# Kernel optimization log

Hardware: AMD Instinct MI355X
Metric: run time of the kernel (lower is better)

The kernel has to match this reference:

```python
import jax, jax.numpy as jnp
import numpy as np
from jax import lax

B, N, C = 4, 3072, 512
SAMPLE_RATIO = 0.25
CLUSTER_NUM = int(np.ceil(N * SAMPLE_RATIO))  # 768, static (mask=None, no 'r')
K = 5  # self.k, since k <= cluster_num


def setup_inputs() -> dict:
    key = jax.random.key(0)
    k1, = jax.random.split(key, 1)
    x = jax.random.normal(k1, (B, N, C), dtype=jnp.float32)
    # idx_token starts as identity mapping per batch (standard TCFormer init)
    idx_token = jnp.tile(jnp.arange(N, dtype=jnp.int32)[None, :], (B, 1))
    agg_weight = jnp.ones((B, N, 1), dtype=jnp.float32)
    return {"x": x, "idx_token": idx_token, "agg_weight": agg_weight}


def _cluster_dpc_knn(x):
    # runs under no_grad in torch -> stop_gradient here
    xs = lax.stop_gradient(x).astype(jnp.float32)
    sq = jnp.sum(xs * xs, axis=-1)  # [B,N]
    d2 = sq[:, :, None] + sq[:, None, :] - 2.0 * jnp.einsum('bnc,bmc->bnm', xs, xs)
    dist = jnp.sqrt(jnp.maximum(d2, 0.0)) / jnp.sqrt(jnp.float32(C))  # cdist / C**0.5
    # k nearest (smallest) distances
    neg_nearest, _ = lax.top_k(-dist, K)
    dist_nearest = -neg_nearest  # [B,N,K]
    density = jnp.exp(-jnp.mean(dist_nearest ** 2, axis=-1))
    density = density + jax.random.uniform(jax.random.key(42), density.shape, dtype=density.dtype) * 1e-6
    mask = (density[:, None, :] > density[:, :, None]).astype(x.dtype)  # [B,N,N]
    dist_max = jnp.max(dist.reshape(B, -1), axis=-1)[:, None, None]
    dist_min = jnp.min(dist * mask + dist_max * (1.0 - mask), axis=-1)  # [B,N]
    score = dist_min * density
    _, index_down = lax.top_k(score, CLUSTER_NUM)  # [B,cluster]
    # gather rows of dist at cluster centers, assign each token to nearest center
    dmat = jnp.take_along_axis(dist, index_down[:, :, None], axis=1)  # [B,cluster,N]
    idx_cluster = jnp.argmin(dmat, axis=1).astype(jnp.int32)  # [B,N]
    # force centers to map to their own cluster id
    idx_cluster = idx_cluster.at[jnp.arange(B)[:, None], index_down].set(
        jnp.broadcast_to(jnp.arange(CLUSTER_NUM, dtype=jnp.int32)[None, :], (B, CLUSTER_NUM)))
    return idx_cluster


def reference(x, idx_token, agg_weight):
    idx_cluster = _cluster_dpc_knn(x)
    # merge_tokens
    token_weight = jnp.ones((B, N, 1), dtype=x.dtype)
    idx = idx_cluster + jnp.arange(B, dtype=jnp.int32)[:, None] * CLUSTER_NUM  # [B,N]
    idx_flat = idx.reshape(-1)
    all_weight = jax.ops.segment_sum(token_weight.reshape(-1), idx_flat,
                                     num_segments=B * CLUSTER_NUM) + 1e-6  # [B*cluster]
    norm_weight = token_weight / all_weight[idx_flat].reshape(B, N, 1)  # [B,N,1]
    x_merged = jax.ops.segment_sum((x * norm_weight).reshape(B * N, C), idx_flat,
                                   num_segments=B * CLUSTER_NUM).reshape(B, CLUSTER_NUM, C)
    idx_token_new = jnp.take_along_axis(idx_cluster, idx_token, axis=1)  # [B,N]
    weight_t = jnp.take_along_axis(norm_weight, idx_token[:, :, None], axis=1)  # [B,N,1]
    agg_weight_new = agg_weight * weight_t
    return x_merged, agg_weight_new, idx_token_new, idx_cluster
```

## Files before the change

### kernel.cpp

```cpp
#include <hip/hip_runtime.h>
#include <math.h>
#include <float.h>

constexpr int B  = 4;
constexpr int N  = 3072;
constexpr int C  = 512;
constexpr int CL = 768;

typedef unsigned short u16;
typedef __attribute__((ext_vector_type(8))) short s16x8;
typedef __attribute__((ext_vector_type(4))) float f32x4;

__device__ __forceinline__ unsigned rotl32(unsigned v, int d) { return (v << d) | (v >> (32 - d)); }

__device__ inline void threefry2x32(unsigned k0, unsigned k1, unsigned c0, unsigned c1,
                                    unsigned& o0, unsigned& o1) {
  unsigned ks0 = k0, ks1 = k1, ks2 = 0x1BD11BDAu ^ k0 ^ k1;
  unsigned x0 = c0 + ks0, x1 = c1 + ks1;
#define TF_RND(r) { x0 += x1; x1 = rotl32(x1, (r)); x1 ^= x0; }
  TF_RND(13) TF_RND(15) TF_RND(26) TF_RND(6)  x0 += ks1; x1 += ks2 + 1u;
  TF_RND(17) TF_RND(29) TF_RND(16) TF_RND(24) x0 += ks2; x1 += ks0 + 2u;
  TF_RND(13) TF_RND(15) TF_RND(26) TF_RND(6)  x0 += ks0; x1 += ks1 + 3u;
  TF_RND(17) TF_RND(29) TF_RND(16) TF_RND(24) x0 += ks1; x1 += ks2 + 4u;
  TF_RND(13) TF_RND(15) TF_RND(26) TF_RND(6)  x0 += ks2; x1 += ks0 + 5u;
#undef TF_RND
  o0 = x0; o1 = x1;
}

__device__ inline float jax_uniform_bn(int f) {
  constexpr int HALF = (B * N) / 2;
  unsigned o0, o1, bits;
  if (f < HALF) { threefry2x32(0u, 42u, (unsigned)f, (unsigned)(f + HALF), o0, o1); bits = o0; }
  else          { threefry2x32(0u, 42u, (unsigned)(f - HALF), (unsigned)f, o0, o1); bits = o1; }
  return __uint_as_float((bits >> 9) | 0x3f800000u) - 1.0f;
}

__device__ __forceinline__ u16 bf16rn(float f) {
  unsigned u = __float_as_uint(f);
  unsigned r = u + 0x7FFFu + ((u >> 16) & 1u);
  return (u16)(r >> 16);
}
__device__ __forceinline__ float bf16tof(u16 h) {
  return __uint_as_float(((unsigned)h) << 16);
}

__global__ __launch_bounds__(64) void k_prep(const float* __restrict__ x, float* __restrict__ sq,
                                             u16* __restrict__ xhi, u16* __restrict__ xlo,
                                             int* __restrict__ counts,
                                             unsigned long long* __restrict__ packed,
                                             float* __restrict__ distmax) {
  int row = blockIdx.x;
  int lane = threadIdx.x;
  const float* xr = x + (size_t)row * C;
  u16* hr = xhi + (size_t)row * C;
  u16* lr = xlo + (size_t)row * C;
  float s = 0.f;
  for (int c = lane * 4; c < C; c += 256) {
    float4 v = *(const float4*)(xr + c);
    s += v.x * v.x + v.y * v.y + v.z * v.z + v.w * v.w;
    u16 h0 = bf16rn(v.x), h1 = bf16rn(v.y), h2 = bf16rn(v.z), h3 = bf16rn(v.w);
    u16 l0 = bf16rn(v.x - bf16tof(h0));
    u16 l1 = bf16rn(v.y - bf16tof(h1));
    u16 l2 = bf16rn(v.z - bf16tof(h2));
    u16 l3 = bf16rn(v.w - bf16tof(h3));
    uint2 hp, lp;
    hp.x = (unsigned)h0 | ((unsigned)h1 << 16); hp.y = (unsigned)h2 | ((unsigned)h3 << 16);
    lp.x = (unsigned)l0 | ((unsigned)l1 << 16); lp.y = (unsigned)l2 | ((unsigned)l3 << 16);
    *(uint2*)(hr + c) = hp;
    *(uint2*)(lr + c) = lp;
  }
  for (int o = 32; o > 0; o >>= 1) s += __shfl_down(s, o, 64);
  if (lane == 0) {
    sq[row] = s;
    packed[row] = ~0ull;
    if (row < B * CL) counts[row] = 0;
    if (row < B) distmax[row] = 0.f;
  }
}

__device__ __forceinline__ void ins5b(float t[5], float v) {
  float c = v;
  float n;
  n = fminf(t[0], c); c = fmaxf(t[0], c); t[0] = n;
  n = fminf(t[1], c); c = fmaxf(t[1], c); t[1] = n;
  n = fminf(t[2], c); c = fmaxf(t[2], c); t[2] = n;
  n = fminf(t[3], c); c = fmaxf(t[3], c); t[3] = n;
  t[4] = fminf(t[4], c);
}

constexpr int NT3 = N / 128;
constexpr int NTILE3 = NT3 * (NT3 + 1) / 2;

__global__ __launch_bounds__(256, 2) void k_distm(const u16* __restrict__ xhi, const u16* __restrict__ xlo,
                                                  const float* __restrict__ sq,
                                                  float* __restrict__ distbuf,
                                                  float* __restrict__ part5, int b0) {
  __shared__ __align__(16) char smem[65536];
  u16* smem_u16 = (u16*)smem;

  int bl = blockIdx.y, b = b0 + bl;

  int bx = blockIdx.x;
  constexpr int NX = 8, QX = NTILE3 / NX, RX = NTILE3 % NX;
  int xcd = bx % NX, sub = bx / NX;
  int idx = (xcd < RX ? xcd * (QX + 1) : RX * (QX + 1) + (xcd - RX) * QX) + sub;

  int ti = 0, rem = idx;
  while (rem >= NT3 - ti) { rem -= NT3 - ti; ++ti; }
  int tj = ti + rem;
  int i0 = ti * 128, j0 = tj * 128;
  bool do_mirror = (ti != tj);

  const float* sqb = sq + (size_t)b * N;
  float* dist = distbuf + (size_t)bl * N * N;

  int tid = threadIdx.x;
  int lane = tid & 63, w = tid >> 6;
  int wr = (w >> 1) * 64, wc = (w & 1) * 64;
  int l15 = lane & 15, l4 = lane >> 4;
  int csw = (lane >> 1) & 3;

  const u16* hil = (w & 1) ? xlo : xhi;
  int rbase0 = (w < 2) ? i0 : j0;
  const u16* gsrc = hil + ((size_t)b * N + rbase0 + (lane >> 2)) * C
                        + ((lane & 3) ^ ((lane >> 3) & 3)) * 8;

  f32x4 acc[4][4];
#pragma unroll
  for (int rt = 0; rt < 4; ++rt)
#pragma unroll
    for (int ct = 0; ct < 4; ++ct)
#pragma unroll
      for (int e = 0; e < 4; ++e) acc[rt][ct][e] = 0.f;

  {
    u16* lb = smem_u16 + w * 4096;
#pragma unroll
    for (int q = 0; q < 8; ++q)
      __builtin_amdgcn_global_load_lds(
          (const __attribute__((address_space(1))) void*)(gsrc + q * 16 * C),
          (__attribute__((address_space(3))) void*)(lb + q * 512), 16, 0, 0);
  }

#define KSTEP(CUR, STG, KNXT, DO_STAGE)                                              \
  {                                                                                  \
    if (DO_STAGE) {                                                                  \
      u16* lb = smem_u16 + (STG) * 16384 + w * 4096;                                 \
      const u16* gs = gsrc + (KNXT);                                                 \
      _Pragma("unroll")                                                              \
      for (int q = 0; q < 8; ++q)                                                    \
        __builtin_amdgcn_global_load_lds(                                            \
            (const __attribute__((address_space(1))) void*)(gs + q * 16 * C),        \
            (__attribute__((address_space(3))) void*)(lb + q * 512), 16, 0, 0);      \
      asm volatile("s_waitcnt vmcnt(8)" ::: "memory");                               \
    } else {                                                                         \
      asm volatile("s_waitcnt vmcnt(0)" ::: "memory");                               \
    }                                                                                \
    __builtin_amdgcn_s_barrier();                                                    \
    asm volatile("" ::: "memory");                                                   \
    const u16* sb = smem_u16 + (CUR) * 16384;                                        \
    s16x8 ah[4], al[4];                                                              \
    _Pragma("unroll")                                                                \
    for (int rt = 0; rt < 4; ++rt) {                                                 \
      int ro = (wr + rt * 16 + l15) * 32 + (l4 ^ csw) * 8;                           \
      ah[rt] = *(const s16x8*)(sb + ro);                                             \
      al[rt] = *(const s16x8*)(sb + 4096 + ro);                                      \
    }                                                                                \
    _Pragma("unroll")                                                                \
    for (int ct = 0; ct < 4; ++ct) {                                                 \
      int co = (wc + ct * 16 + l15) * 32 + (l4 ^ csw) * 8;                           \
      s16x8 bh = *(const s16x8*)(sb + 8192 + co);                                    \
      s16x8 bl = *(const s16x8*)(sb + 12288 + co);                                   \
      _Pragma("unroll")                                                              \
      for (int rt = 0; rt < 4; ++rt) {                                               \
        acc[rt][ct] = __builtin_amdgcn_mfma_f32_16x16x32_bf16(ah[rt], bh, acc[rt][ct], 0, 0, 0); \
        acc[rt][ct] = __builtin_amdgcn_mfma_f32_16x16x32_bf16(ah[rt], bl, acc[rt][ct], 0, 0, 0); \
        acc[rt][ct] = __builtin_amdgcn_mfma_f32_16x16x32_bf16(al[rt], bh, acc[rt][ct], 0, 0, 0); \
      }                                                                              \
    }                                                                                \
    asm volatile("" ::: "memory");                                                   \
    __builtin_amdgcn_s_barrier();                                                    \
    asm volatile("" ::: "memory");                                                   \
  }

  for (int ks = 0; ks < 16; ks += 2) {
    KSTEP(0, 1, (ks + 1) * 32, true)
    KSTEP(1, 0, (ks + 2) * 32, (ks + 2 < 16))
  }
#undef KSTEP

  const float SQC = 22.627416997969522f;
  float sqi[4][4], sqj[4];
#pragma unroll
  for (int rt = 0; rt < 4; ++rt)
#pragma unroll
    for (int r = 0; r < 4; ++r) sqi[rt][r] = sqb[i0 + wr + rt * 16 + l4 * 4 + r];
#pragma unroll
  for (int ct = 0; ct < 4; ++ct) sqj[ct] = sqb[j0 + wc + ct * 16 + l15];

#pragma unroll
  for (int rt = 0; rt < 4; ++rt)
#pragma unroll
    for (int ct = 0; ct < 4; ++ct)
#pragma unroll
      for (int r = 0; r < 4; ++r) {
        float d2 = fmaxf(sqi[rt][r] + sqj[ct] - 2.0f * acc[rt][ct][r], 0.0f);
        acc[rt][ct][r] = sqrtf(d2) / SQC;
      }

  constexpr int TSTR = 77;
  float* sT = (float*)smem + w * (32 * TSTR);

  float t5A[5] = {FLT_MAX, FLT_MAX, FLT_MAX, FLT_MAX, FLT_MAX};
  float mxA = 0.f;

#pragma unroll
  for (int p = 0; p < 2; ++p) {
#pragma unroll
    for (int cth = 0; cth < 2; ++cth) {
      int ct = p * 2 + cth;
      int cl = cth * 16 + l15;
#pragma unroll
      for (int rt = 0; rt < 4; ++rt)
#pragma unroll
        for (int r = 0; r < 4; ++r)
          sT[cl * TSTR + rt * 16 + l4 * 4 + r] = acc[rt][ct][r];
    }
    {
      int g4 = lane & 7, rbase = lane >> 3;
#pragma unroll
      for (int it = 0; it < 8; ++it) {
        int rl = it * 8 + rbase;
        float4 v = make_float4(sT[(4 * g4 + 0) * TSTR + rl],
                               sT[(4 * g4 + 1) * TSTR + rl],
                               sT[(4 * g4 + 2) * TSTR + rl],
                               sT[(4 * g4 + 3) * TSTR + rl]);
        *(float4*)(dist + (size_t)(i0 + wr + rl) * N + j0 + wc + p * 32 + 4 * g4) = v;
      }
    }
    if (do_mirror) {
      int cg = lane >> 4, rq = lane & 15;
#pragma unroll
      for (int cc = 0; cc < 8; ++cc) {
        int c = cc * 4 + cg;
        float4 v;
        v.x = sT[c * TSTR + rq * 4 + 0];
        v.y = sT[c * TSTR + rq * 4 + 1];
        v.z = sT[c * TSTR + rq * 4 + 2];
        v.w = sT[c * TSTR + rq * 4 + 3];
        *(float4*)(dist + (size_t)(j0 + wc + p * 32 + c) * N + i0 + wr + rq * 4) = v;
      }
    }
    for (int c = 0; c < 32; ++c) {
      float v = sT[c * TSTR + lane];
      mxA = fmaxf(mxA, v);
      ins5b(t5A, v);
    }
    if (do_mirror) {
      int cl = lane & 31, half = lane >> 5;
      float t5B[5] = {FLT_MAX, FLT_MAX, FLT_MAX, FLT_MAX, FLT_MAX};
      float mxB = 0.f;
      for (int k = 0; k < 32; ++k) {
        float v = sT[cl * TSTR + half * 32 + k];
        mxB = fmaxf(mxB, v);
        ins5b(t5B, v);
      }
      mxB = fmaxf(mxB, __shfl_xor(mxB, 32, 64));
      float o0 = __shfl_xor(t5B[0], 32, 64);
      float o1 = __shfl_xor(t5B[1], 32, 64);
      float o2 = __shfl_xor(t5B[2], 32, 64);
      float o3 = __shfl_xor(t5B[3], 32, 64);
      float o4 = __shfl_xor(t5B[4], 32, 64);
      ins5b(t5B, o0); ins5b(t5B, o1); ins5b(t5B, o2); ins5b(t5B, o3); ins5b(t5B, o4);
      if (half == 0) {
        int rowB = j0 + wc + p * 32 + cl;
        int slotB = ti * 2 + (wr >> 6);
        float* dst = part5 + (((size_t)bl * 48 + slotB) * 6) * N + rowB;
        dst[0] = t5B[0]; dst[(size_t)N] = t5B[1]; dst[2 * (size_t)N] = t5B[2];
        dst[3 * (size_t)N] = t5B[3]; dst[4 * (size_t)N] = t5B[4]; dst[5 * (size_t)N] = mxB;
      }
    }
  }
  {
    int rowA = i0 + wr + lane;
    int slotA = tj * 2 + (wc >> 6);
    float* dst = part5 + (((size_t)bl * 48 + slotA) * 6) * N + rowA;
    dst[0] = t5A[0]; dst[(size_t)N] = t5A[1]; dst[2 * (size_t)N] = t5A[2];
    dst[3 * (size_t)N] = t5A[3]; dst[4 * (size_t)N] = t5A[4]; dst[5 * (size_t)N] = mxA;
  }
}

__global__ __launch_bounds__(256) void k_dens(const float* __restrict__ part5,
                                              float* __restrict__ density,
                                              float* __restrict__ distmax, int b0) {
  int g = blockIdx.x * 256 + threadIdx.x;
  int bl = g / N, r = g % N;
  int b = b0 + bl;
  const float* base = part5 + (size_t)bl * 48 * 6 * N + r;
  float t5[5] = {FLT_MAX, FLT_MAX, FLT_MAX, FLT_MAX, FLT_MAX};
  float mx = 0.f;
  for (int s = 0; s < 48; ++s) {
    const float* sp = base + (size_t)s * 6 * N;
    ins5b(t5, sp[0]);
    ins5b(t5, sp[(size_t)N]);
    ins5b(t5, sp[2 * (size_t)N]);
    ins5b(t5, sp[3 * (size_t)N]);
    ins5b(t5, sp[4 * (size_t)N]);
    mx = fmaxf(mx, sp[5 * (size_t)N]);
  }
  float sum = t5[0] * t5[0] + t5[1] * t5[1] + t5[2] * t5[2] + t5[3] * t5[3] + t5[4] * t5[4];
  density[b * N + r] = expf(-(sum / 5.0f)) + jax_uniform_bn(b * N + r) * 1e-6f;
#pragma unroll
  for (int m = 1; m < 64; m <<= 1) mx = fmaxf(mx, __shfl_xor(mx, m, 64));
  if ((threadIdx.x & 63) == 0) atomicMax((int*)(distmax + b), __float_as_int(mx));
}

__global__ __launch_bounds__(256) void k_maskmin(const float* __restrict__ distbuf,
                                                 const float* __restrict__ density,
                                                 const float* __restrict__ distmax,
                                                 float* __restrict__ score, int b0) {
  __shared__ float sd[N];
  int tid = threadIdx.x;
  int wv = tid >> 6, lane = tid & 63;
  int bl = blockIdx.y, b = b0 + bl;
  const float* db = density + (size_t)b * N;
  for (int j = tid * 4; j < N; j += 1024) *(float4*)(sd + j) = *(const float4*)(db + j);
  __syncthreads();
  int i0r = blockIdx.x * 16 + wv * 4;
  float dmax = distmax[b];
  const float* row0 = distbuf + ((size_t)bl * N + i0r) * N;
  float di0 = sd[i0r], di1 = sd[i0r + 1], di2 = sd[i0r + 2], di3 = sd[i0r + 3];
  float mn0 = dmax, mn1 = dmax, mn2 = dmax, mn3 = dmax;
#pragma unroll 2
  for (int it = 0; it < N / 256; ++it) {
    int j = it * 256 + lane * 4;
    float4 d  = *(const float4*)(sd + j);
    float4 v0 = *(const float4*)(row0 + j);
    float4 v1 = *(const float4*)(row0 + (size_t)N + j);
    float4 v2 = *(const float4*)(row0 + 2 * (size_t)N + j);
    float4 v3 = *(const float4*)(row0 + 3 * (size_t)N + j);
    mn0 = fminf(mn0, (d.x > di0) ? v0.x : dmax);
    mn0 = fminf(mn0, (d.y > di0) ? v0.y : dmax);
    mn0 = fminf(mn0, (d.z > di0) ? v0.z : dmax);
    mn0 = fminf(mn0, (d.w > di0) ? v0.w : dmax);
    mn1 = fminf(mn1, (d.x > di1) ? v1.x : dmax);
    mn1 = fminf(mn1, (d.y > di1) ? v1.y : dmax);
    mn1 = fminf(mn1, (d.z > di1) ? v1.z : dmax);
    mn1 = fminf(mn1, (d.w > di1) ? v1.w : dmax);
    mn2 = fminf(mn2, (d.x > di2) ? v2.x : dmax);
    mn2 = fminf(mn2, (d.y > di2) ? v2.y : dmax);
    mn2 = fminf(mn2, (d.z > di2) ? v2.z : dmax);
    mn2 = fminf(mn2, (d.w > di2) ? v2.w : dmax);
    mn3 = fminf(mn3, (d.x > di3) ? v3.x : dmax);
    mn3 = fminf(mn3, (d.y > di3) ? v3.y : dmax);
    mn3 = fminf(mn3, (d.z > di3) ? v3.z : dmax);
    mn3 = fminf(mn3, (d.w > di3) ? v3.w : dmax);
  }
#pragma unroll
  for (int m = 1; m < 64; m <<= 1) {
    mn0 = fminf(mn0, __shfl_xor(mn0, m, 64));
    mn1 = fminf(mn1, __shfl_xor(mn1, m, 64));
    mn2 = fminf(mn2, __shfl_xor(mn2, m, 64));
    mn3 = fminf(mn3, __shfl_xor(mn3, m, 64));
  }
  if (lane == 0) {
    score[b * N + i0r]     = mn0 * di0;
    score[b * N + i0r + 1] = mn1 * di1;
    score[b * N + i0r + 2] = mn2 * di2;
    score[b * N + i0r + 3] = mn3 * di3;
  }
}

__global__ __launch_bounds__(256) void k_rank(const float* __restrict__ score,
                                              int* __restrict__ index_down,
                                              int* __restrict__ rank, int b0) {
  __shared__ float ssc[N];
  int tid = threadIdx.x;
  int wv = tid >> 6, lane = tid & 63;
  int b = b0 + blockIdx.y;
  const float* sb = score + (size_t)b * N;
  for (int j = tid * 4; j < N; j += 1024) *(float4*)(ssc + j) = *(const float4*)(sb + j);
  __syncthreads();
  int i0r = blockIdx.x * 16 + wv * 4;
  float s0 = ssc[i0r], s1 = ssc[i0r + 1], s2 = ssc[i0r + 2], s3 = ssc[i0r + 3];
  int c0 = 0, c1 = 0, c2 = 0, c3 = 0;
#pragma unroll 2
  for (int it = 0; it < N / 256; ++it) {
    int j = it * 256 + lane * 4;
    float4 v = *(const float4*)(ssc + j);
    c0 += (v.x > s0) || (v.x == s0 && (j + 0) < i0r);
    c0 += (v.y > s0) || (v.y == s0 && (j + 1) < i0r);
    c0 += (v.z > s0) || (v.z == s0 && (j + 2) < i0r);
    c0 += (v.w > s0) || (v.w == s0 && (j + 3) < i0r);
    c1 += (v.x > s1) || (v.x == s1 && (j + 0) < i0r + 1);
    c1 += (v.y > s1) || (v.y == s1 && (j + 1) < i0r + 1);
    c1 += (v.z > s1) || (v.z == s1 && (j + 2) < i0r + 1);
    c1 += (v.w > s1) || (v.w == s1 && (j + 3) < i0r + 1);
    c2 += (v.x > s2) || (v.x == s2 && (j + 0) < i0r + 2);
    c2 += (v.y > s2) || (v.y == s2 && (j + 1) < i0r + 2);
    c2 += (v.z > s2) || (v.z == s2 && (j + 2) < i0r + 2);
    c2 += (v.w > s2) || (v.w == s2 && (j + 3) < i0r + 2);
    c3 += (v.x > s3) || (v.x == s3 && (j + 0) < i0r + 3);
    c3 += (v.y > s3) || (v.y == s3 && (j + 1) < i0r + 3);
    c3 += (v.z > s3) || (v.z == s3 && (j + 2) < i0r + 3);
    c3 += (v.w > s3) || (v.w == s3 && (j + 3) < i0r + 3);
  }
#pragma unroll
  for (int m = 1; m < 64; m <<= 1) {
    c0 += __shfl_xor(c0, m, 64);
    c1 += __shfl_xor(c1, m, 64);
    c2 += __shfl_xor(c2, m, 64);
    c3 += __shfl_xor(c3, m, 64);
  }
  if (lane == 0) {
    rank[b * N + i0r]     = (c0 < CL) ? c0 : -1;
    rank[b * N + i0r + 1] = (c1 < CL) ? c1 : -1;
    rank[b * N + i0r + 2] = (c2 < CL) ? c2 : -1;
    rank[b * N + i0r + 3] = (c3 < CL) ? c3 : -1;
    if (c0 < CL) index_down[b * CL + c0] = i0r;
    if (c1 < CL) index_down[b * CL + c1] = i0r + 1;
    if (c2 < CL) index_down[b * CL + c2] = i0r + 2;
    if (c3 < CL) index_down[b * CL + c3] = i0r + 3;
  }
}

__global__ __launch_bounds__(256) void k_assign_part(const float* __restrict__ distbuf,
                                                     const int* __restrict__ index_down,
                                                     unsigned long long* __restrict__ packed, int b0) {
  constexpr int RCH = CL / 8;
  __shared__ int sid[RCH];
  int bl = blockIdx.z, b = b0 + bl;
  int r0 = blockIdx.y * RCH;
  int tid = threadIdx.x;
  for (int r = tid; r < RCH; r += 256) sid[r] = index_down[b * CL + r0 + r];
  __syncthreads();
  int j = blockIdx.x * 256 + tid;
  const float* base = distbuf + (size_t)bl * N * N;
  float best = FLT_MAX; int bestr = 0;
#pragma unroll 8
  for (int r = 0; r < RCH; ++r) {
    float d = base[(size_t)sid[r] * N + j];
    if (d < best) { best = d; bestr = r0 + r; }
  }
  unsigned long long key = ((unsigned long long)__float_as_uint(best) << 32) | (unsigned)bestr;
  atomicMin(&packed[b * N + j], key);
}

__global__ void k_assign_fin2(const unsigned long long* __restrict__ packed,
                              const int* __restrict__ rank,
                              int* __restrict__ idx_cluster, int* __restrict__ counts) {
  int g = blockIdx.x * 256 + threadIdx.x;
  int b = g / N;
  int r = rank[g];
  int cl = (r >= 0) ? r : (int)(unsigned)(packed[g] & 0xffffffffull);
  idx_cluster[g] = cl;
  atomicAdd(&counts[b * CL + cl], 1);
}

__global__ __launch_bounds__(1024) void k_scan(const int* __restrict__ counts,
                                               int* __restrict__ offsets, int* __restrict__ cursor) {
  constexpr int T = B * CL;
  __shared__ int sm[T];
  int tid = threadIdx.x;
  for (int p = tid; p < T; p += 1024) sm[p] = counts[p];
  __syncthreads();
  for (int off = 1; off < T; off <<= 1) {
    int v[3]; int n = 0;
    for (int p = tid; p < T; p += 1024) { v[n++] = (p >= off) ? sm[p - off] : 0; }
    __syncthreads();
    n = 0;
    for (int p = tid; p < T; p += 1024) { sm[p] += v[n++]; }
    __syncthreads();
  }
  for (int p = tid; p < T; p += 1024) {
    int e = sm[p] - counts[p];
    offsets[p] = e; cursor[p] = e;
  }
}

__global__ void k_fill(const int* __restrict__ idx_cluster, int* __restrict__ cursor,
                       int* __restrict__ members) {
  int g = blockIdx.x * 256 + threadIdx.x;
  int b = g / N, i = g % N;
  int seg = b * CL + idx_cluster[g];
  int pos = atomicAdd(&cursor[seg], 1);
  members[pos] = i;
}

__global__ __launch_bounds__(128) void k_gather(const float* __restrict__ x, const int* __restrict__ members,
                                                const int* __restrict__ offsets, const int* __restrict__ counts,
                                                float* __restrict__ out0) {
  int seg = blockIdx.x;
  int b = seg / CL;
  int cnt = counts[seg], off = offsets[seg];
  float nw = 1.0f / ((float)cnt + 1e-6f);
  int c = threadIdx.x * 4;
  const float* xb = x + (size_t)b * N * C;
  float4 acc = make_float4(0.f, 0.f, 0.f, 0.f);
  for (int m = 0; m < cnt; ++m) {
    int tok = members[off + m];
    float4 v = *(const float4*)(xb + (size_t)tok * C + c);
    acc.x += v.x * nw; acc.y += v.y * nw; acc.z += v.z * nw; acc.w += v.w * nw;
  }
  *(float4*)(out0 + (size_t)seg * C + c) = acc;
}

__global__ void k_final(const float* __restrict__ agg_weight, const int* __restrict__ idx_token,
                        const int* __restrict__ idx_cluster, const int* __restrict__ counts,
                        float* __restrict__ out1, float* __restrict__ out2, float* __restrict__ out3) {
  int g = blockIdx.x * 256 + threadIdx.x;
  int b = g / N;
  int it = idx_token[g];
  int clt = idx_cluster[b * N + it];
  float nwt = 1.0f / ((float)counts[b * CL + clt] + 1e-6f);
  out1[g] = agg_weight[g] * nwt;
  out2[g] = (float)clt;
  out3[g] = (float)idx_cluster[g];
}

extern "C" void kernel_launch(void* const* d_in, const int* in_sizes, int n_in,
                              void* d_out, int out_size, void* d_ws, size_t ws_size,
                              hipStream_t stream) {
  const float* x          = (const float*)d_in[0];
  const int*   idx_token  = (const int*)d_in[1];
  const float* agg_weight = (const float*)d_in[2];

  float* out0 = (float*)d_out;
  float* out1 = out0 + (size_t)B * CL * C;
  float* out2 = out1 + (size_t)B * N;
  float* out3 = out2 + (size_t)B * N;

  char* w = (char*)d_ws;
  auto carve = [&](size_t bytes) { char* p = w; w += (bytes + 255) & ~(size_t)255; return p; };
  float*    sq         = (float*)carve((size_t)B * N * 4);
  float*    density    = (float*)carve((size_t)B * N * 4);
  float*    score      = (float*)carve((size_t)B * N * 4);
  float*    distmax    = (float*)carve((size_t)B * 4);
  int*      index_down = (int*)carve((size_t)B * CL * 4);
  int*      rank       = (int*)carve((size_t)B * N * 4);
  int*      idx_clus   = (int*)carve((size_t)B * N * 4);
  int*      counts     = (int*)carve((size_t)B * CL * 4);
  int*      offsets    = (int*)carve((size_t)B * CL * 4);
  int*      cursor     = (int*)carve((size_t)B * CL * 4);
  int*      members    = (int*)carve((size_t)B * N * 4);
  unsigned long long* packed = (unsigned long long*)carve((size_t)B * N * 8);
  u16*      xhi        = (u16*)carve((size_t)B * N * C * 2);
  u16*      xlo        = (u16*)carve((size_t)B * N * C * 2);
  float*    part5      = (float*)carve((size_t)B * 48 * 6 * N * 4);
  size_t used = (size_t)(w - (char*)d_ws);
  size_t per  = (size_t)N * N * 4;
  int nb_max = (ws_size > used) ? (int)((ws_size - used) / per) : 0;
  if (nb_max < 1) nb_max = 1;
  if (nb_max > B) nb_max = B;
  float* distbuf = (float*)w;

  k_prep<<<B * N, 64, 0, stream>>>(x, sq, xhi, xlo, counts, packed, distmax);

  for (int b0 = 0; b0 < B; b0 += nb_max) {
    int nb = (B - b0 < nb_max) ? (B - b0) : nb_max;
    k_distm<<<dim3(NTILE3, nb), 256, 0, stream>>>(xhi, xlo, sq, distbuf, part5, b0);
    k_dens<<<(nb * N) / 256, 256, 0, stream>>>(part5, density, distmax, b0);
    k_maskmin<<<dim3(N / 16, nb), 256, 0, stream>>>(distbuf, density, distmax, score, b0);
    k_rank<<<dim3(N / 16, nb), 256, 0, stream>>>(score, index_down, rank, b0);
    k_assign_part<<<dim3(N / 256, 8, nb), 256, 0, stream>>>(distbuf, index_down, packed, b0);
  }

  k_assign_fin2<<<(B * N) / 256, 256, 0, stream>>>(packed, rank, idx_clus, counts);
  k_scan<<<1, 1024, 0, stream>>>(counts, offsets, cursor);
  k_fill<<<(B * N) / 256, 256, 0, stream>>>(idx_clus, cursor, members);
  k_gather<<<B * CL, 128, 0, stream>>>(x, members, offsets, counts, out0);
  k_final<<<(B * N) / 256, 256, 0, stream>>>(agg_weight, idx_token, idx_clus, counts, out1, out2, out3);
}
```

Baseline: 293.3 us.

## Load A operands directly from global and halve LDS to raise occupancy

The distance GEMM kernel no longer stages the A-side (row) hi/lo bf16 tiles through LDS. Each wave now reads its A fragments straight from global memory into registers at the start of every k-step, and only the B-side tiles are double-buffered in LDS with half the async loads and a matching vmcnt. This cuts the LDS footprint so the launch bound can ask for 4 blocks per CU instead of 2, aiming to hide latency through occupancy. In exchange, A reads rely on L1/L2 hits (two waves share the same rows), register pressure rises under the tighter launch bound, and sched_barriers fix the instruction order around the MFMA block.

```diff
diff --git a/kernel.cpp b/kernel.cpp
--- a/kernel.cpp
+++ b/kernel.cpp
@@ -91,11 +91,11 @@
 constexpr int NT3 = N / 128;
 constexpr int NTILE3 = NT3 * (NT3 + 1) / 2;
 
-__global__ __launch_bounds__(256, 2) void k_distm(const u16* __restrict__ xhi, const u16* __restrict__ xlo,
+__global__ __launch_bounds__(256, 4) void k_distm(const u16* __restrict__ xhi, const u16* __restrict__ xlo,
                                                   const float* __restrict__ sq,
                                                   float* __restrict__ distbuf,
                                                   float* __restrict__ part5, int b0) {
-  __shared__ __align__(16) char smem[65536];
+  __shared__ __align__(16) char smem[39424];
   u16* smem_u16 = (u16*)smem;
 
   int bl = blockIdx.y, b = b0 + bl;
@@ -120,10 +120,15 @@
   int l15 = lane & 15, l4 = lane >> 4;
   int csw = (lane >> 1) & 3;
 
-  const u16* hil = (w & 1) ? xlo : xhi;
-  int rbase0 = (w < 2) ? i0 : j0;
-  const u16* gsrc = hil + ((size_t)b * N + rbase0 + (lane >> 2)) * C
-                        + ((lane & 3) ^ ((lane >> 3) & 3)) * 8;
+  const u16* hilB = (w < 2) ? xhi : xlo;
+  const u16* gsrcB = hilB + ((size_t)b * N + j0 + (w & 1) * 64 + (lane >> 2)) * C
+                          + ((lane & 3) ^ ((lane >> 3) & 3)) * 8;
+  int ldsB = w * 2048;
+
+  size_t aoff[4];
+#pragma unroll
+  for (int rt = 0; rt < 4; ++rt)
+    aoff[rt] = ((size_t)b * N + i0 + wr + rt * 16 + l15) * C + l4 * 8;
 
   f32x4 acc[4][4];
 #pragma unroll
@@ -134,43 +139,42 @@
       for (int e = 0; e < 4; ++e) acc[rt][ct][e] = 0.f;
 
   {
-    u16* lb = smem_u16 + w * 4096;
-#pragma unroll
-    for (int q = 0; q < 8; ++q)
+#pragma unroll
+    for (int q = 0; q < 4; ++q)
       __builtin_amdgcn_global_load_lds(
-          (const __attribute__((address_space(1))) void*)(gsrc + q * 16 * C),
-          (__attribute__((address_space(3))) void*)(lb + q * 512), 16, 0, 0);
-  }
-
-#define KSTEP(CUR, STG, KNXT, DO_STAGE)                                              \
+          (const __attribute__((address_space(1))) void*)(gsrcB + q * 16 * C),
+          (__attribute__((address_space(3))) void*)(smem_u16 + ldsB + q * 512), 16, 0, 0);
+  }
+
+#define KSTEP(CUR, STG, K0A, KNXT, DO_STAGE)                                         \
   {                                                                                  \
+    s16x8 ah[4], al[4];                                                              \
+    _Pragma("unroll")                                                                \
+    for (int rt = 0; rt < 4; ++rt) {                                                 \
+      ah[rt] = *(const s16x8*)(xhi + aoff[rt] + (K0A));                              \
+      al[rt] = *(const s16x8*)(xlo + aoff[rt] + (K0A));                              \
+    }                                                                                \
     if (DO_STAGE) {                                                                  \
-      u16* lb = smem_u16 + (STG) * 16384 + w * 4096;                                 \
-      const u16* gs = gsrc + (KNXT);                                                 \
+      const u16* gs = gsrcB + (KNXT);                                                \
+      u16* lb = smem_u16 + (STG) * 8192 + ldsB;                                      \
       _Pragma("unroll")                                                              \
-      for (int q = 0; q < 8; ++q)                                                    \
+      for (int q = 0; q < 4; ++q)                                                    \
         __builtin_amdgcn_global_load_lds(                                            \
             (const __attribute__((address_space(1))) void*)(gs + q * 16 * C),        \
             (__attribute__((address_space(3))) void*)(lb + q * 512), 16, 0, 0);      \
-      asm volatile("s_waitcnt vmcnt(8)" ::: "memory");                               \
+      asm volatile("s_waitcnt vmcnt(4)" ::: "memory");                               \
     } else {                                                                         \
       asm volatile("s_waitcnt vmcnt(0)" ::: "memory");                               \
     }                                                                                \
     __builtin_amdgcn_s_barrier();                                                    \
     asm volatile("" ::: "memory");                                                   \
-    const u16* sb = smem_u16 + (CUR) * 16384;                                        \
-    s16x8 ah[4], al[4];                                                              \
-    _Pragma("unroll")                                                                \
-    for (int rt = 0; rt < 4; ++rt) {                                                 \
-      int ro = (wr + rt * 16 + l15) * 32 + (l4 ^ csw) * 8;                           \
-      ah[rt] = *(const s16x8*)(sb + ro);                                             \
-      al[rt] = *(const s16x8*)(sb + 4096 + ro);                                      \
-    }                                                                                \
+    __builtin_amdgcn_sched_barrier(0);                                               \
+    const u16* sb = smem_u16 + (CUR) * 8192;                                         \
     _Pragma("unroll")                                                                \
     for (int ct = 0; ct < 4; ++ct) {                                                 \
       int co = (wc + ct * 16 + l15) * 32 + (l4 ^ csw) * 8;                           \
-      s16x8 bh = *(const s16x8*)(sb + 8192 + co);                                    \
-      s16x8 bl = *(const s16x8*)(sb + 12288 + co);                                   \
+      s16x8 bh = *(const s16x8*)(sb + co);                                           \
+      s16x8 bl = *(const s16x8*)(sb + 4096 + co);                                    \
       _Pragma("unroll")                                                              \
       for (int rt = 0; rt < 4; ++rt) {                                               \
         acc[rt][ct] = __builtin_amdgcn_mfma_f32_16x16x32_bf16(ah[rt], bh, acc[rt][ct], 0, 0, 0); \
@@ -178,14 +182,15 @@
         acc[rt][ct] = __builtin_amdgcn_mfma_f32_16x16x32_bf16(al[rt], bh, acc[rt][ct], 0, 0, 0); \
       }                                                                              \
     }                                                                                \
+    __builtin_amdgcn_sched_barrier(0);                                               \
     asm volatile("" ::: "memory");                                                   \
     __builtin_amdgcn_s_barrier();                                                    \
     asm volatile("" ::: "memory");                                                   \
   }
 
   for (int ks = 0; ks < 16; ks += 2) {
-    KSTEP(0, 1, (ks + 1) * 32, true)
-    KSTEP(1, 0, (ks + 2) * 32, (ks + 2 < 16))
+    KSTEP(0, 1, ks * 32, (ks + 1) * 32, true)
+    KSTEP(1, 0, (ks + 1) * 32, (ks + 2) * 32, (ks + 2 < 16))
   }
 #undef KSTEP
 
```

After: 395.3 us. +34.8%, slower.
